# Optimization experiments

Measured on AMD Instinct MI355X. Metric: run time of the kernel, lower is better.

## Reference

```python
import jax, jax.numpy as jnp
import numpy as np

B, C, O, K, H, W = 32, 256, 256, 7, 31, 31


def _unfold(x, k):
    """Extract kxk sliding windows (stride 1, no padding, no dilation).

    x: [B, C, H, W] -> patches [B, C, k, k, Ho, Wo]
    """
    _, _, h, w = x.shape
    ho, wo = h - k + 1, w - k + 1
    # fixed small loop over k*k window offsets (k=7 -> 49 cheap slices)
    rows = []
    for i in range(k):
        cols = [x[:, :, i:i + ho, j:j + wo] for j in range(k)]
        rows.append(jnp.stack(cols, axis=2))  # [B, C, k, Ho, Wo]
    return jnp.stack(rows, axis=2)  # [B, C, k, k, Ho, Wo]


def setup_inputs() -> dict:
    key = jax.random.key(0)
    k1, k2, k3, k4 = jax.random.split(key, 4)
    x = jax.random.normal(k1, (B, C, H, W), dtype=jnp.float32)
    kernel = jax.random.normal(k2, (B, C, K, K), dtype=jnp.float32)
    weight = jax.random.normal(k3, (O, C, K, K), dtype=jnp.float32) * 0.02
    bias = jax.random.normal(k4, (O,), dtype=jnp.float32) * 0.02
    return {"x": x, "kernel": kernel, "weight": weight, "bias": bias}


def reference(x, kernel, weight, bias):
    k = weight.shape[-1]
    patches = _unfold(x, k)  # [B, C, k, k, Ho, Wo]
    # fused: (patches * kernel[..., None, None]) contracted with weight
    # torch: einsum('ijklmn,ojkl->iomn', patches * kernel_view, weight)
    out = jnp.einsum('bcklhw,bckl,ockl->bohw', patches, kernel, weight)
    out = out + bias[None, :, None, None]
    return out
```

## Files before the change

### kernel.cpp

```cpp
#include <hip/hip_runtime.h>
#include <hip/hip_fp16.h>

typedef _Float16 half8 __attribute__((ext_vector_type(8)));
typedef __attribute__((ext_vector_type(4)))  float floatx4;
typedef __attribute__((ext_vector_type(16))) float floatx16;

#define BB 32
#define CC 256
#define OO 256
#define KS 7
#define HH 31
#define WW 31
#define HO 25
#define PP 625
#define SS 49

#define SLAB_PITCH 40
#define SLAB_ROWS  310
#define P_TILE 64
#define NPX 10
#define KPD 20

#define WT4_ELEMS  ((size_t)SS * 8 * 2 * CC * 16)
#define WT4_BYTES  (WT4_ELEMS * 2)

static __device__ __forceinline__ unsigned pk2h(float lo, float hi) {
    __half2 h = __floats2half2_rn(lo, hi);
    unsigned r;
    __builtin_memcpy(&r, &h, sizeof(r));
    return r;
}
static __device__ __forceinline__ unsigned mulh2(unsigned a, unsigned b) {
    __half2 x, y;
    __builtin_memcpy(&x, &a, 4); __builtin_memcpy(&y, &b, 4);
    __half2 r = __hmul2(x, y);
    unsigned u;
    __builtin_memcpy(&u, &r, 4);
    return u;
}
static __device__ __forceinline__ half8 mod8(uint4 w, uint4 k) {
    uint4 r;
    r.x = mulh2(w.x, k.x); r.y = mulh2(w.y, k.y);
    r.z = mulh2(w.z, k.z); r.w = mulh2(w.w, k.w);
    return __builtin_bit_cast(half8, r);
}

__global__ __launch_bounds__(256) void repack_w(const float* __restrict__ w,
                                                unsigned short* __restrict__ wt4) {
    const int bid = blockIdx.x;
    const int s = bid >> 3, cb = bid & 7;
    const int o = threadIdx.x;
    const float* src = w + ((size_t)o * CC + cb * 32) * SS + s;
    float v[32];
#pragma unroll
    for (int ci = 0; ci < 32; ++ci) v[ci] = src[(size_t)ci * SS];
#pragma unroll
    for (int kh = 0; kh < 2; ++kh) {
        unsigned short* dst = wt4 + ((size_t)bid * 2 + kh) * (CC * 16) + o * 16;
        uint4 p0, p1;
        p0.x = pk2h(v[kh*16+0], v[kh*16+1]);  p0.y = pk2h(v[kh*16+2], v[kh*16+3]);
        p0.z = pk2h(v[kh*16+4], v[kh*16+5]);  p0.w = pk2h(v[kh*16+6], v[kh*16+7]);
        p1.x = pk2h(v[kh*16+8], v[kh*16+9]);  p1.y = pk2h(v[kh*16+10], v[kh*16+11]);
        p1.z = pk2h(v[kh*16+12], v[kh*16+13]); p1.w = pk2h(v[kh*16+14], v[kh*16+15]);
        *(uint4*)(dst)     = p0;
        *(uint4*)(dst + 8) = p1;
    }
}

__global__ __launch_bounds__(256, 4) void dwconv_fused(
        const float* __restrict__ x, const unsigned short* __restrict__ wt4,
        const float* __restrict__ kern, const float* __restrict__ bias,
        float* __restrict__ out) {
    __shared__ unsigned short slab[SLAB_ROWS * SLAB_PITCH];
    __shared__ unsigned klds[SS * KPD];

    const int tid = threadIdx.x;
    const int id = blockIdx.x;
    const int oy = id & 1;
    const int m = id >> 1;
    const int b = m / NPX, px = m - (m / NPX) * NPX;

    const int p0 = px * P_TILE;
    const int h0 = p0 / HO;
    const int pmax = (p0 + P_TILE - 1 < PP - 1) ? p0 + P_TILE - 1 : PP - 1;
    const int rows = pmax / HO - h0 + 7;
    const int npos = rows * WW;

    const int lane = tid & 63, wid = tid >> 6;
    const int l32 = lane & 31, half = lane >> 5;

    int bOff[2];
#pragma unroll
    for (int ph = 0; ph < 2; ++ph) {
        int p = p0 + ph * 32 + l32;
        if (p > PP - 1) p = PP - 1;
        int h = p / HO, ww_ = p - h * HO;
        bOff[ph] = ((h - h0) * WW + ww_) * SLAB_PITCH + half * 8;
    }

    const unsigned short* wbase = wt4
        + (size_t)(oy * 128 + wid * 32 + l32) * 16 + half * 8;

    floatx16 acc[2];
#pragma unroll
    for (int ph = 0; ph < 2; ++ph)
#pragma unroll
        for (int rr = 0; rr < 16; ++rr) acc[ph][rr] = 0.f;

    for (int cb = 0; cb < 8; ++cb) {
        __syncthreads();
        {
            const float* xsrc = x + ((size_t)(b * CC + cb * 32 + wid * 8)) * (HH * WW)
                                  + h0 * WW;
#pragma unroll
            for (int it = 0; it < 5; ++it) {
                int pos = lane + it * 64;
                if (pos < npos) {
                    float v[8];
#pragma unroll
                    for (int j = 0; j < 8; ++j) v[j] = xsrc[j * (HH * WW) + pos];
                    uint4 pkt;
                    pkt.x = pk2h(v[0], v[1]); pkt.y = pk2h(v[2], v[3]);
                    pkt.z = pk2h(v[4], v[5]); pkt.w = pk2h(v[6], v[7]);
                    *(uint4*)(slab + pos * SLAB_PITCH + wid * 8) = pkt;
                }
            }
        }
        {
            const float* ksrc = kern + ((size_t)(b * CC + cb * 32)) * SS;
#pragma unroll
            for (int it = 0; it < 4; ++it) {
                int f = tid + it * 256;
                if (f < 16 * SS) {
                    int s = f >> 4, pr = f & 15;
                    float v0 = ksrc[(size_t)(pr * 2) * SS + s];
                    float v1 = ksrc[(size_t)(pr * 2 + 1) * SS + s];
                    klds[s * KPD + pr] = pk2h(v0, v1);
                }
            }
        }
        __syncthreads();

        const unsigned short* aptr = wbase + (size_t)cb * 8192;
        uint4 a0k0 = *(const uint4*)(aptr);
        uint4 a0k1 = *(const uint4*)(aptr + 4096);
        uint4 a1k0 = *(const uint4*)(aptr + 65536);
        uint4 a1k1 = *(const uint4*)(aptr + 65536 + 4096);

        int kk = 0, ll = 0;
        for (int si = 0; si < SS; ++si) {
            uint4 n0, n1;
            if (si + 2 < SS) {
                const unsigned short* p2 = aptr + 2 * 65536;
                n0 = *(const uint4*)(p2);
                n1 = *(const uint4*)(p2 + 4096);
            } else {
                n0 = a1k0; n1 = a1k1;
            }

            uint4 kv0 = *(const uint4*)(klds + si * KPD + half * 4);
            uint4 kv1 = *(const uint4*)(klds + si * KPD + 8 + half * 4);

            const unsigned short* slabS = slab + (kk * WW + ll) * SLAB_PITCH;
            half8 b00 = *(const half8*)(slabS + bOff[0]);
            half8 b01 = *(const half8*)(slabS + bOff[0] + 16);
            half8 b10 = *(const half8*)(slabS + bOff[1]);
            half8 b11 = *(const half8*)(slabS + bOff[1] + 16);

            half8 a0 = mod8(a0k0, kv0);
            half8 a1 = mod8(a0k1, kv1);

            acc[0] = __builtin_amdgcn_mfma_f32_32x32x16_f16(a0, b00, acc[0], 0, 0, 0);
            acc[1] = __builtin_amdgcn_mfma_f32_32x32x16_f16(a0, b10, acc[1], 0, 0, 0);
            acc[0] = __builtin_amdgcn_mfma_f32_32x32x16_f16(a1, b01, acc[0], 0, 0, 0);
            acc[1] = __builtin_amdgcn_mfma_f32_32x32x16_f16(a1, b11, acc[1], 0, 0, 0);

            a0k0 = a1k0; a0k1 = a1k1; a1k0 = n0; a1k1 = n1;
            aptr += 65536;
            if (++ll == KS) { ll = 0; ++kk; }
        }
    }

    const int ow0 = oy * 128 + wid * 32;
#pragma unroll
    for (int c = 0; c < 4; ++c) {
        const int ob = ow0 + c * 8 + 4 * half;
        const float4 bv = *(const float4*)(bias + ob);
#pragma unroll
        for (int ph = 0; ph < 2; ++ph) {
            const int p = p0 + ph * 32 + l32;
            if (p < PP) {
                out[((size_t)(b * OO + ob + 0)) * PP + p] = acc[ph][4*c+0] + bv.x;
                out[((size_t)(b * OO + ob + 1)) * PP + p] = acc[ph][4*c+1] + bv.y;
                out[((size_t)(b * OO + ob + 2)) * PP + p] = acc[ph][4*c+2] + bv.z;
                out[((size_t)(b * OO + ob + 3)) * PP + p] = acc[ph][4*c+3] + bv.w;
            }
        }
    }
}

__global__ __launch_bounds__(256) void dwconv_naive(
        const float* __restrict__ x, const float* __restrict__ kern,
        const float* __restrict__ w, const float* __restrict__ bias,
        float* __restrict__ out) {
    const int idx = blockIdx.x * 256 + threadIdx.x;
    if (idx >= BB * OO * PP) return;
    const int p = idx % PP;
    const int o = (idx / PP) % OO;
    const int b = idx / (PP * OO);
    const int h = p / HO;
    const int wq = p - h * HO;
    float acc = 0.f;
    for (int c = 0; c < CC; ++c) {
        const float* xp = x + ((size_t)(b * CC + c)) * (HH * WW) + h * WW + wq;
        const float* kp = kern + ((size_t)b * CC + c) * SS;
        const float* wp = w + ((size_t)o * CC + c) * SS;
#pragma unroll
        for (int s = 0; s < SS; ++s) {
            const int kk = s / KS;
            const int ll = s - kk * KS;
            acc += xp[kk * WW + ll] * kp[s] * wp[s];
        }
    }
    out[idx] = acc + bias[o];
}

extern "C" void kernel_launch(void* const* d_in, const int* in_sizes, int n_in,
                              void* d_out, int out_size, void* d_ws, size_t ws_size,
                              hipStream_t stream) {
    const float* x    = (const float*)d_in[0];
    const float* kern = (const float*)d_in[1];
    const float* w    = (const float*)d_in[2];
    const float* bias = (const float*)d_in[3];
    float* out = (float*)d_out;

    if (ws_size >= WT4_BYTES) {
        unsigned short* wt4 = (unsigned short*)d_ws;
        repack_w<<<dim3(SS * 8), dim3(256), 0, stream>>>(w, wt4);
        dwconv_fused<<<dim3(640), dim3(256), 0, stream>>>(x, wt4, kern, bias, out);
    } else {
        const int total = BB * OO * PP;
        dwconv_naive<<<dim3((total + 255) / 256), dim3(256), 0, stream>>>(
            x, kern, w, bias, out);
    }
}
```

Before: 292.8 us.

## Split the 49 kernel taps across wave groups with an LDS reduction, using 512-thread blocks

Blocks grow to 512 threads (8 waves). Each wave covers 64 outputs by 32 pixels instead of 32 by 64, and the 49 spatial taps are split between two wave groups (25 and 24). A two-round LDS reduction then combines the partial accumulators before the bias add and store. The slab pitch shrinks to 36 and the weight register prefetch pipeline is removed. The aim is more waves in flight and shorter serial MFMA chains, at the cost of an extra reduction, more barriers, and no weight prefetch (weights are now loaded directly each tap).

```diff
diff --git a/kernel.cpp b/kernel.cpp
--- a/kernel.cpp
+++ b/kernel.cpp
@@ -15,7 +15,7 @@
 #define PP 625
 #define SS 49
 
-#define SLAB_PITCH 40
+#define SLAB_PITCH 36
 #define SLAB_ROWS  310
 #define P_TILE 64
 #define NPX 10
@@ -67,7 +67,7 @@
     }
 }
 
-__global__ __launch_bounds__(256, 4) void dwconv_fused(
+__global__ __launch_bounds__(512, 6) void dwconv_fused(
         const float* __restrict__ x, const unsigned short* __restrict__ wt4,
         const float* __restrict__ kern, const float* __restrict__ bias,
         float* __restrict__ out) {
@@ -87,50 +87,53 @@
     const int npos = rows * WW;
 
     const int lane = tid & 63, wid = tid >> 6;
+    const int wo = wid & 1, wp = (wid >> 1) & 1, kw = wid >> 2;
     const int l32 = lane & 31, half = lane >> 5;
 
-    int bOff[2];
-#pragma unroll
-    for (int ph = 0; ph < 2; ++ph) {
-        int p = p0 + ph * 32 + l32;
+    int bOff;
+    {
+        int p = p0 + wp * 32 + l32;
         if (p > PP - 1) p = PP - 1;
         int h = p / HO, ww_ = p - h * HO;
-        bOff[ph] = ((h - h0) * WW + ww_) * SLAB_PITCH + half * 8;
-    }
+        bOff = ((h - h0) * WW + ww_) * SLAB_PITCH + half * 8;
+    }
+
+    const int s0 = kw ? 25 : 0;
+    const int ns = kw ? 24 : 25;
 
     const unsigned short* wbase = wt4
-        + (size_t)(oy * 128 + wid * 32 + l32) * 16 + half * 8;
+        + (size_t)(oy * 128 + wo * 64 + l32) * 16 + half * 8;
 
     floatx16 acc[2];
 #pragma unroll
-    for (int ph = 0; ph < 2; ++ph)
-#pragma unroll
-        for (int rr = 0; rr < 16; ++rr) acc[ph][rr] = 0.f;
+    for (int oh = 0; oh < 2; ++oh)
+#pragma unroll
+        for (int rr = 0; rr < 16; ++rr) acc[oh][rr] = 0.f;
 
     for (int cb = 0; cb < 8; ++cb) {
         __syncthreads();
         {
-            const float* xsrc = x + ((size_t)(b * CC + cb * 32 + wid * 8)) * (HH * WW)
+            const float* xsrc = x + ((size_t)(b * CC + cb * 32 + wid * 4)) * (HH * WW)
                                   + h0 * WW;
 #pragma unroll
             for (int it = 0; it < 5; ++it) {
                 int pos = lane + it * 64;
                 if (pos < npos) {
-                    float v[8];
-#pragma unroll
-                    for (int j = 0; j < 8; ++j) v[j] = xsrc[j * (HH * WW) + pos];
-                    uint4 pkt;
-                    pkt.x = pk2h(v[0], v[1]); pkt.y = pk2h(v[2], v[3]);
-                    pkt.z = pk2h(v[4], v[5]); pkt.w = pk2h(v[6], v[7]);
-                    *(uint4*)(slab + pos * SLAB_PITCH + wid * 8) = pkt;
+                    float v0 = xsrc[pos];
+                    float v1 = xsrc[(size_t)(HH * WW) + pos];
+                    float v2 = xsrc[(size_t)(2 * HH * WW) + pos];
+                    float v3 = xsrc[(size_t)(3 * HH * WW) + pos];
+                    uint2 pkt;
+                    pkt.x = pk2h(v0, v1); pkt.y = pk2h(v2, v3);
+                    *(uint2*)(slab + pos * SLAB_PITCH + wid * 4) = pkt;
                 }
             }
         }
         {
             const float* ksrc = kern + ((size_t)(b * CC + cb * 32)) * SS;
 #pragma unroll
-            for (int it = 0; it < 4; ++it) {
-                int f = tid + it * 256;
+            for (int it = 0; it < 2; ++it) {
+                int f = tid + it * 512;
                 if (f < 16 * SS) {
                     int s = f >> 4, pr = f & 15;
                     float v0 = ksrc[(size_t)(pr * 2) * SS + s];
@@ -141,60 +144,69 @@
         }
         __syncthreads();
 
-        const unsigned short* aptr = wbase + (size_t)cb * 8192;
-        uint4 a0k0 = *(const uint4*)(aptr);
-        uint4 a0k1 = *(const uint4*)(aptr + 4096);
-        uint4 a1k0 = *(const uint4*)(aptr + 65536);
-        uint4 a1k1 = *(const uint4*)(aptr + 65536 + 4096);
-
-        int kk = 0, ll = 0;
-        for (int si = 0; si < SS; ++si) {
-            uint4 n0, n1;
-            if (si + 2 < SS) {
-                const unsigned short* p2 = aptr + 2 * 65536;
-                n0 = *(const uint4*)(p2);
-                n1 = *(const uint4*)(p2 + 4096);
-            } else {
-                n0 = a1k0; n1 = a1k1;
-            }
-
-            uint4 kv0 = *(const uint4*)(klds + si * KPD + half * 4);
-            uint4 kv1 = *(const uint4*)(klds + si * KPD + 8 + half * 4);
+        const unsigned short* aptr = wbase + (size_t)(s0 * 8 + cb) * 8192;
+
+        int kk = kw ? 3 : 0, ll = kw ? 4 : 0;
+        for (int si = 0; si < ns; ++si) {
+            uint4 wa0 = *(const uint4*)(aptr);
+            uint4 wa1 = *(const uint4*)(aptr + 512);
+            uint4 wa2 = *(const uint4*)(aptr + 4096);
+            uint4 wa3 = *(const uint4*)(aptr + 4608);
+
+            const unsigned* kp = klds + (size_t)(s0 + si) * KPD;
+            uint4 kv0 = *(const uint4*)(kp + half * 4);
+            uint4 kv1 = *(const uint4*)(kp + 8 + half * 4);
 
             const unsigned short* slabS = slab + (kk * WW + ll) * SLAB_PITCH;
-            half8 b00 = *(const half8*)(slabS + bOff[0]);
-            half8 b01 = *(const half8*)(slabS + bOff[0] + 16);
-            half8 b10 = *(const half8*)(slabS + bOff[1]);
-            half8 b11 = *(const half8*)(slabS + bOff[1] + 16);
-
-            half8 a0 = mod8(a0k0, kv0);
-            half8 a1 = mod8(a0k1, kv1);
-
-            acc[0] = __builtin_amdgcn_mfma_f32_32x32x16_f16(a0, b00, acc[0], 0, 0, 0);
-            acc[1] = __builtin_amdgcn_mfma_f32_32x32x16_f16(a0, b10, acc[1], 0, 0, 0);
-            acc[0] = __builtin_amdgcn_mfma_f32_32x32x16_f16(a1, b01, acc[0], 0, 0, 0);
-            acc[1] = __builtin_amdgcn_mfma_f32_32x32x16_f16(a1, b11, acc[1], 0, 0, 0);
-
-            a0k0 = a1k0; a0k1 = a1k1; a1k0 = n0; a1k1 = n1;
+            half8 b0 = *(const half8*)(slabS + bOff);
+            half8 b1 = *(const half8*)(slabS + bOff + 16);
+
+            half8 a0 = mod8(wa0, kv0);
+            half8 a1 = mod8(wa1, kv0);
+            half8 a2 = mod8(wa2, kv1);
+            half8 a3 = mod8(wa3, kv1);
+
+            acc[0] = __builtin_amdgcn_mfma_f32_32x32x16_f16(a0, b0, acc[0], 0, 0, 0);
+            acc[1] = __builtin_amdgcn_mfma_f32_32x32x16_f16(a1, b0, acc[1], 0, 0, 0);
+            acc[0] = __builtin_amdgcn_mfma_f32_32x32x16_f16(a2, b1, acc[0], 0, 0, 0);
+            acc[1] = __builtin_amdgcn_mfma_f32_32x32x16_f16(a3, b1, acc[1], 0, 0, 0);
+
             aptr += 65536;
             if (++ll == KS) { ll = 0; ++kk; }
         }
     }
 
-    const int ow0 = oy * 128 + wid * 32;
-#pragma unroll
-    for (int c = 0; c < 4; ++c) {
-        const int ob = ow0 + c * 8 + 4 * half;
-        const float4 bv = *(const float4*)(bias + ob);
-#pragma unroll
-        for (int ph = 0; ph < 2; ++ph) {
-            const int p = p0 + ph * 32 + l32;
-            if (p < PP) {
-                out[((size_t)(b * OO + ob + 0)) * PP + p] = acc[ph][4*c+0] + bv.x;
-                out[((size_t)(b * OO + ob + 1)) * PP + p] = acc[ph][4*c+1] + bv.y;
-                out[((size_t)(b * OO + ob + 2)) * PP + p] = acc[ph][4*c+2] + bv.z;
-                out[((size_t)(b * OO + ob + 3)) * PP + p] = acc[ph][4*c+3] + bv.w;
-            }
+    float* red = (float*)slab;
+    for (int round = 0; round < 2; ++round) {
+        __syncthreads();
+        if (kw == 1 && wp == round) {
+#pragma unroll
+            for (int oh = 0; oh < 2; ++oh)
+#pragma unroll
+                for (int c = 0; c < 4; ++c) {
+                    floatx4 v4 = {acc[oh][4*c+0], acc[oh][4*c+1],
+                                  acc[oh][4*c+2], acc[oh][4*c+3]};
+                    *(floatx4*)(red + wo * 2176 + l32 * 68 + oh * 32 + c * 8 + 4 * half) = v4;
+                }
+        }
+        __syncthreads();
+        if (kw == 0 && wp == round) {
+            const int pout = p0 + wp * 32 + l32;
+#pragma unroll
+            for (int oh = 0; oh < 2; ++oh)
+#pragma unroll
+                for (int c = 0; c < 4; ++c) {
+                    const int ob = oy * 128 + wo * 64 + oh * 32 + c * 8 + 4 * half;
+                    const float4 bv = *(const float4*)(bias + ob);
+                    floatx4 v4 = *(const floatx4*)(red + wo * 2176 + l32 * 68
+                                                   + oh * 32 + c * 8 + 4 * half);
+                    if (pout < PP) {
+                        out[((size_t)(b * OO + ob + 0)) * PP + pout] = acc[oh][4*c+0] + v4[0] + bv.x;
+                        out[((size_t)(b * OO + ob + 1)) * PP + pout] = acc[oh][4*c+1] + v4[1] + bv.y;
+                        out[((size_t)(b * OO + ob + 2)) * PP + pout] = acc[oh][4*c+2] + v4[2] + bv.z;
+                        out[((size_t)(b * OO + ob + 3)) * PP + pout] = acc[oh][4*c+3] + v4[3] + bv.w;
+                    }
+                }
         }
     }
 }
@@ -237,7 +249,7 @@
     if (ws_size >= WT4_BYTES) {
         unsigned short* wt4 = (unsigned short*)d_ws;
         repack_w<<<dim3(SS * 8), dim3(256), 0, stream>>>(w, wt4);
-        dwconv_fused<<<dim3(640), dim3(256), 0, stream>>>(x, wt4, kern, bias, out);
+        dwconv_fused<<<dim3(640), dim3(512), 0, stream>>>(x, wt4, kern, bias, out);
     } else {
         const int total = BB * OO * PP;
         dwconv_naive<<<dim3((total + 255) / 256), dim3(256), 0, stream>>>(
```

Result: slower. 414.7 us (+41.6%).

## Retile conv to 128-pixel by 32-output blocks and pre-pack x to fp16

Applied to the files above, without the earlier changes.

Adds a pack_x pre-pass that converts x to fp16 in workspace, so the main kernel loads half-width data and skips the per-block conversion. The block tile changes from 64 pixels × 128 outputs (two accumulators per wave) to 128 pixels × 32 outputs (one accumulator per wave), with 1280 blocks and a larger, narrower-pitch slab. The aim is more blocks and higher occupancy from fewer registers. The cost is an extra kernel launch, extra x traffic through workspace, and more redundant staging of x and kern because eight output tiles now each load the same slab.

```diff
diff --git a/kernel.cpp b/kernel.cpp
--- a/kernel.cpp
+++ b/kernel.cpp
@@ -15,14 +15,16 @@
 #define PP 625
 #define SS 49
 
-#define SLAB_PITCH 40
-#define SLAB_ROWS  310
-#define P_TILE 64
-#define NPX 10
+#define SLAB_PITCH 36
+#define SLAB_ROWS  372
+#define P_TILE 128
+#define NPX 5
 #define KPD 20
 
 #define WT4_ELEMS  ((size_t)SS * 8 * 2 * CC * 16)
 #define WT4_BYTES  (WT4_ELEMS * 2)
+#define X16_ELEMS  ((size_t)BB * CC * HH * WW)
+#define X16_BYTES  (X16_ELEMS * 2)
 
 static __device__ __forceinline__ unsigned pk2h(float lo, float hi) {
     __half2 h = __floats2half2_rn(lo, hi);
@@ -67,8 +69,18 @@
     }
 }
 
-__global__ __launch_bounds__(256, 4) void dwconv_fused(
-        const float* __restrict__ x, const unsigned short* __restrict__ wt4,
+__global__ __launch_bounds__(256) void pack_x(const float* __restrict__ x,
+                                              unsigned short* __restrict__ x16) {
+    const size_t i4 = ((size_t)blockIdx.x * 256 + threadIdx.x) * 4;
+    float4 v = *(const float4*)(x + i4);
+    uint2 p;
+    p.x = pk2h(v.x, v.y); p.y = pk2h(v.z, v.w);
+    *(uint2*)(x16 + i4) = p;
+}
+
+__global__ __launch_bounds__(256, 5) void dwconv_fused(
+        const unsigned short* __restrict__ x16,
+        const unsigned short* __restrict__ wt4,
         const float* __restrict__ kern, const float* __restrict__ bias,
         float* __restrict__ out) {
     __shared__ unsigned short slab[SLAB_ROWS * SLAB_PITCH];
@@ -76,8 +88,8 @@
 
     const int tid = threadIdx.x;
     const int id = blockIdx.x;
-    const int oy = id & 1;
-    const int m = id >> 1;
+    const int oy = id & 7;
+    const int m = id >> 3;
     const int b = m / NPX, px = m - (m / NPX) * NPX;
 
     const int p0 = px * P_TILE;
@@ -89,39 +101,37 @@
     const int lane = tid & 63, wid = tid >> 6;
     const int l32 = lane & 31, half = lane >> 5;
 
-    int bOff[2];
-#pragma unroll
-    for (int ph = 0; ph < 2; ++ph) {
-        int p = p0 + ph * 32 + l32;
+    int bOff;
+    {
+        int p = p0 + wid * 32 + l32;
         if (p > PP - 1) p = PP - 1;
         int h = p / HO, ww_ = p - h * HO;
-        bOff[ph] = ((h - h0) * WW + ww_) * SLAB_PITCH + half * 8;
-    }
-
-    const unsigned short* wbase = wt4
-        + (size_t)(oy * 128 + wid * 32 + l32) * 16 + half * 8;
-
-    floatx16 acc[2];
-#pragma unroll
-    for (int ph = 0; ph < 2; ++ph)
-#pragma unroll
-        for (int rr = 0; rr < 16; ++rr) acc[ph][rr] = 0.f;
+        bOff = ((h - h0) * WW + ww_) * SLAB_PITCH + half * 8;
+    }
+
+    const unsigned short* wbase = wt4 + (size_t)(oy * 32 + l32) * 16 + half * 8;
+
+    floatx16 acc;
+#pragma unroll
+    for (int rr = 0; rr < 16; ++rr) acc[rr] = 0.f;
 
     for (int cb = 0; cb < 8; ++cb) {
         __syncthreads();
         {
-            const float* xsrc = x + ((size_t)(b * CC + cb * 32 + wid * 8)) * (HH * WW)
-                                  + h0 * WW;
-#pragma unroll
-            for (int it = 0; it < 5; ++it) {
+            const unsigned short* xsrc = x16
+                + ((size_t)(b * CC + cb * 32 + wid * 8)) * (HH * WW) + h0 * WW;
+#pragma unroll
+            for (int it = 0; it < 6; ++it) {
                 int pos = lane + it * 64;
                 if (pos < npos) {
-                    float v[8];
+                    unsigned short v[8];
 #pragma unroll
                     for (int j = 0; j < 8; ++j) v[j] = xsrc[j * (HH * WW) + pos];
                     uint4 pkt;
-                    pkt.x = pk2h(v[0], v[1]); pkt.y = pk2h(v[2], v[3]);
-                    pkt.z = pk2h(v[4], v[5]); pkt.w = pk2h(v[6], v[7]);
+                    pkt.x = (unsigned)v[0] | ((unsigned)v[1] << 16);
+                    pkt.y = (unsigned)v[2] | ((unsigned)v[3] << 16);
+                    pkt.z = (unsigned)v[4] | ((unsigned)v[5] << 16);
+                    pkt.w = (unsigned)v[6] | ((unsigned)v[7] << 16);
                     *(uint4*)(slab + pos * SLAB_PITCH + wid * 8) = pkt;
                 }
             }
@@ -158,22 +168,19 @@
                 n0 = a1k0; n1 = a1k1;
             }
 
-            uint4 kv0 = *(const uint4*)(klds + si * KPD + half * 4);
-            uint4 kv1 = *(const uint4*)(klds + si * KPD + 8 + half * 4);
+            const unsigned* kp = klds + (size_t)si * KPD;
+            uint4 kv0 = *(const uint4*)(kp + half * 4);
+            uint4 kv1 = *(const uint4*)(kp + 8 + half * 4);
 
             const unsigned short* slabS = slab + (kk * WW + ll) * SLAB_PITCH;
-            half8 b00 = *(const half8*)(slabS + bOff[0]);
-            half8 b01 = *(const half8*)(slabS + bOff[0] + 16);
-            half8 b10 = *(const half8*)(slabS + bOff[1]);
-            half8 b11 = *(const half8*)(slabS + bOff[1] + 16);
+            half8 b0 = *(const half8*)(slabS + bOff);
+            half8 b1 = *(const half8*)(slabS + bOff + 16);
 
             half8 a0 = mod8(a0k0, kv0);
             half8 a1 = mod8(a0k1, kv1);
 
-            acc[0] = __builtin_amdgcn_mfma_f32_32x32x16_f16(a0, b00, acc[0], 0, 0, 0);
-            acc[1] = __builtin_amdgcn_mfma_f32_32x32x16_f16(a0, b10, acc[1], 0, 0, 0);
-            acc[0] = __builtin_amdgcn_mfma_f32_32x32x16_f16(a1, b01, acc[0], 0, 0, 0);
-            acc[1] = __builtin_amdgcn_mfma_f32_32x32x16_f16(a1, b11, acc[1], 0, 0, 0);
+            acc = __builtin_amdgcn_mfma_f32_32x32x16_f16(a0, b0, acc, 0, 0, 0);
+            acc = __builtin_amdgcn_mfma_f32_32x32x16_f16(a1, b1, acc, 0, 0, 0);
 
             a0k0 = a1k0; a0k1 = a1k1; a1k0 = n0; a1k1 = n1;
             aptr += 65536;
@@ -181,20 +188,16 @@
         }
     }
 
-    const int ow0 = oy * 128 + wid * 32;
-#pragma unroll
-    for (int c = 0; c < 4; ++c) {
-        const int ob = ow0 + c * 8 + 4 * half;
-        const float4 bv = *(const float4*)(bias + ob);
-#pragma unroll
-        for (int ph = 0; ph < 2; ++ph) {
-            const int p = p0 + ph * 32 + l32;
-            if (p < PP) {
-                out[((size_t)(b * OO + ob + 0)) * PP + p] = acc[ph][4*c+0] + bv.x;
-                out[((size_t)(b * OO + ob + 1)) * PP + p] = acc[ph][4*c+1] + bv.y;
-                out[((size_t)(b * OO + ob + 2)) * PP + p] = acc[ph][4*c+2] + bv.z;
-                out[((size_t)(b * OO + ob + 3)) * PP + p] = acc[ph][4*c+3] + bv.w;
-            }
+    const int pout = p0 + wid * 32 + l32;
+    if (pout < PP) {
+#pragma unroll
+        for (int c = 0; c < 4; ++c) {
+            const int ob = oy * 32 + c * 8 + 4 * half;
+            const float4 bv = *(const float4*)(bias + ob);
+            out[((size_t)(b * OO + ob + 0)) * PP + pout] = acc[4*c+0] + bv.x;
+            out[((size_t)(b * OO + ob + 1)) * PP + pout] = acc[4*c+1] + bv.y;
+            out[((size_t)(b * OO + ob + 2)) * PP + pout] = acc[4*c+2] + bv.z;
+            out[((size_t)(b * OO + ob + 3)) * PP + pout] = acc[4*c+3] + bv.w;
         }
     }
 }
@@ -234,10 +237,12 @@
     const float* bias = (const float*)d_in[3];
     float* out = (float*)d_out;
 
-    if (ws_size >= WT4_BYTES) {
+    if (ws_size >= WT4_BYTES + X16_BYTES) {
         unsigned short* wt4 = (unsigned short*)d_ws;
+        unsigned short* x16 = (unsigned short*)((char*)d_ws + WT4_BYTES);
         repack_w<<<dim3(SS * 8), dim3(256), 0, stream>>>(w, wt4);
-        dwconv_fused<<<dim3(640), dim3(256), 0, stream>>>(x, wt4, kern, bias, out);
+        pack_x<<<dim3((unsigned)(X16_ELEMS / 4 / 256)), dim3(256), 0, stream>>>(x, x16);
+        dwconv_fused<<<dim3(1280), dim3(256), 0, stream>>>(x16, wt4, kern, bias, out);
     } else {
         const int total = BB * OO * PP;
         dwconv_naive<<<dim3((total + 255) / 256), dim3(256), 0, stream>>>(
```

Measured after the change: 582.5 us. 98.9% more time.

## Split 49 kernel taps across waves with LDS reduction and 64-output tiles

Applied to the files above, without the earlier changes.

Each block now covers 64 outputs × 64 positions, and its four waves split the 49 spatial taps (13/12/12/12) instead of splitting output channels. Partial accumulators are combined through a serialized LDS reduction before the bias add and store. The grid doubles to 1280 blocks, the block order is swizzled, the slab pitch shrinks to 36, and the occupancy hint drops to 3. This trades extra LDS reduction, barriers and accumulator registers for more parallelism and shared slab reads per weight fragment.

```diff
diff --git a/kernel.cpp b/kernel.cpp
--- a/kernel.cpp
+++ b/kernel.cpp
@@ -15,10 +15,8 @@
 #define PP 625
 #define SS 49
 
-#define SLAB_PITCH 40
+#define SLAB_PITCH 36
 #define SLAB_ROWS  310
-#define P_TILE 64
-#define NPX 10
 #define KPD 20
 
 #define WT4_ELEMS  ((size_t)SS * 8 * 2 * CC * 16)
@@ -67,7 +65,7 @@
     }
 }
 
-__global__ __launch_bounds__(256, 4) void dwconv_fused(
+__global__ __launch_bounds__(256, 3) void dwconv_fused(
         const float* __restrict__ x, const unsigned short* __restrict__ wt4,
         const float* __restrict__ kern, const float* __restrict__ bias,
         float* __restrict__ out) {
@@ -76,17 +74,18 @@
 
     const int tid = threadIdx.x;
     const int id = blockIdx.x;
-    const int oy = id & 1;
-    const int m = id >> 1;
-    const int b = m / NPX, px = m - (m / NPX) * NPX;
-
-    const int p0 = px * P_TILE;
+    const int hi = id / 80, rem = id % 80;
+    const int px = rem >> 3;
+    const int g = hi * 8 + (rem & 7);
+    const int b = g >> 2, oy = g & 3;
+
+    const int p0 = px * 64, o0 = oy * 64;
     const int h0 = p0 / HO;
-    const int pmax = (p0 + P_TILE - 1 < PP - 1) ? p0 + P_TILE - 1 : PP - 1;
+    const int pmax = (p0 + 63 < PP - 1) ? p0 + 63 : PP - 1;
     const int rows = pmax / HO - h0 + 7;
     const int npos = rows * WW;
 
-    const int lane = tid & 63, wid = tid >> 6;
+    const int lane = tid & 63, kw = tid >> 6;
     const int l32 = lane & 31, half = lane >> 5;
 
     int bOff[2];
@@ -98,19 +97,23 @@
         bOff[ph] = ((h - h0) * WW + ww_) * SLAB_PITCH + half * 8;
     }
 
-    const unsigned short* wbase = wt4
-        + (size_t)(oy * 128 + wid * 32 + l32) * 16 + half * 8;
-
-    floatx16 acc[2];
-#pragma unroll
-    for (int ph = 0; ph < 2; ++ph)
-#pragma unroll
-        for (int rr = 0; rr < 16; ++rr) acc[ph][rr] = 0.f;
+    const int s0 = kw * 12 + (kw > 0 ? 1 : 0);
+    const int ns = kw ? 12 : 13;
+
+    const unsigned short* wbase = wt4 + (size_t)(o0 + l32) * 16 + half * 8;
+
+    floatx16 acc[2][2];
+#pragma unroll
+    for (int oh = 0; oh < 2; ++oh)
+#pragma unroll
+        for (int ph = 0; ph < 2; ++ph)
+#pragma unroll
+            for (int r = 0; r < 16; ++r) acc[oh][ph][r] = 0.f;
 
     for (int cb = 0; cb < 8; ++cb) {
         __syncthreads();
         {
-            const float* xsrc = x + ((size_t)(b * CC + cb * 32 + wid * 8)) * (HH * WW)
+            const float* xsrc = x + ((size_t)(b * CC + cb * 32 + kw * 8)) * (HH * WW)
                                   + h0 * WW;
 #pragma unroll
             for (int it = 0; it < 5; ++it) {
@@ -122,7 +125,7 @@
                     uint4 pkt;
                     pkt.x = pk2h(v[0], v[1]); pkt.y = pk2h(v[2], v[3]);
                     pkt.z = pk2h(v[4], v[5]); pkt.w = pk2h(v[6], v[7]);
-                    *(uint4*)(slab + pos * SLAB_PITCH + wid * 8) = pkt;
+                    *(uint4*)(slab + pos * SLAB_PITCH + kw * 8) = pkt;
                 }
             }
         }
@@ -141,61 +144,119 @@
         }
         __syncthreads();
 
-        const unsigned short* aptr = wbase + (size_t)cb * 8192;
-        uint4 a0k0 = *(const uint4*)(aptr);
-        uint4 a0k1 = *(const uint4*)(aptr + 4096);
-        uint4 a1k0 = *(const uint4*)(aptr + 65536);
-        uint4 a1k1 = *(const uint4*)(aptr + 65536 + 4096);
-
-        int kk = 0, ll = 0;
-        for (int si = 0; si < SS; ++si) {
-            uint4 n0, n1;
-            if (si + 2 < SS) {
-                const unsigned short* p2 = aptr + 2 * 65536;
-                n0 = *(const uint4*)(p2);
-                n1 = *(const uint4*)(p2 + 4096);
+        const unsigned short* aptr = wbase + (size_t)(s0 * 8 + cb) * 8192;
+
+        uint4 wa0 = *(const uint4*)(aptr);
+        uint4 wa1 = *(const uint4*)(aptr + 512);
+        uint4 wa2 = *(const uint4*)(aptr + 4096);
+        uint4 wa3 = *(const uint4*)(aptr + 4608);
+
+        int s = s0, kk = s0 / KS, ll = s0 - (s0 / KS) * KS;
+        for (int si = 0; si < ns; ++si) {
+            uint4 wn0, wn1, wn2, wn3;
+            if (si + 1 < ns) {
+                aptr += 65536;
+                wn0 = *(const uint4*)(aptr);
+                wn1 = *(const uint4*)(aptr + 512);
+                wn2 = *(const uint4*)(aptr + 4096);
+                wn3 = *(const uint4*)(aptr + 4608);
             } else {
-                n0 = a1k0; n1 = a1k1;
+                wn0 = wa0; wn1 = wa1; wn2 = wa2; wn3 = wa3;
             }
 
-            uint4 kv0 = *(const uint4*)(klds + si * KPD + half * 4);
-            uint4 kv1 = *(const uint4*)(klds + si * KPD + 8 + half * 4);
+            const unsigned* kp = klds + (size_t)s * KPD;
+            uint4 kv0 = *(const uint4*)(kp + half * 4);
+            uint4 kv1 = *(const uint4*)(kp + 8 + half * 4);
 
             const unsigned short* slabS = slab + (kk * WW + ll) * SLAB_PITCH;
-            half8 b00 = *(const half8*)(slabS + bOff[0]);
-            half8 b01 = *(const half8*)(slabS + bOff[0] + 16);
-            half8 b10 = *(const half8*)(slabS + bOff[1]);
-            half8 b11 = *(const half8*)(slabS + bOff[1] + 16);
-
-            half8 a0 = mod8(a0k0, kv0);
-            half8 a1 = mod8(a0k1, kv1);
-
-            acc[0] = __builtin_amdgcn_mfma_f32_32x32x16_f16(a0, b00, acc[0], 0, 0, 0);
-            acc[1] = __builtin_amdgcn_mfma_f32_32x32x16_f16(a0, b10, acc[1], 0, 0, 0);
-            acc[0] = __builtin_amdgcn_mfma_f32_32x32x16_f16(a1, b01, acc[0], 0, 0, 0);
-            acc[1] = __builtin_amdgcn_mfma_f32_32x32x16_f16(a1, b11, acc[1], 0, 0, 0);
-
-            a0k0 = a1k0; a0k1 = a1k1; a1k0 = n0; a1k1 = n1;
-            aptr += 65536;
-            if (++ll == KS) { ll = 0; ++kk; }
+            half8 sb00 = *(const half8*)(slabS + bOff[0]);
+            half8 sb01 = *(const half8*)(slabS + bOff[0] + 16);
+            half8 sb10 = *(const half8*)(slabS + bOff[1]);
+            half8 sb11 = *(const half8*)(slabS + bOff[1] + 16);
+
+            half8 a00 = mod8(wa0, kv0);
+            half8 a10 = mod8(wa1, kv0);
+            half8 a01 = mod8(wa2, kv1);
+            half8 a11 = mod8(wa3, kv1);
+
+            acc[0][0] = __builtin_amdgcn_mfma_f32_32x32x16_f16(a00, sb00, acc[0][0], 0, 0, 0);
+            acc[0][1] = __builtin_amdgcn_mfma_f32_32x32x16_f16(a00, sb10, acc[0][1], 0, 0, 0);
+            acc[1][0] = __builtin_amdgcn_mfma_f32_32x32x16_f16(a10, sb00, acc[1][0], 0, 0, 0);
+            acc[1][1] = __builtin_amdgcn_mfma_f32_32x32x16_f16(a10, sb10, acc[1][1], 0, 0, 0);
+            acc[0][0] = __builtin_amdgcn_mfma_f32_32x32x16_f16(a01, sb01, acc[0][0], 0, 0, 0);
+            acc[0][1] = __builtin_amdgcn_mfma_f32_32x32x16_f16(a01, sb11, acc[0][1], 0, 0, 0);
+            acc[1][0] = __builtin_amdgcn_mfma_f32_32x32x16_f16(a11, sb01, acc[1][0], 0, 0, 0);
+            acc[1][1] = __builtin_amdgcn_mfma_f32_32x32x16_f16(a11, sb11, acc[1][1], 0, 0, 0);
+
+            wa0 = wn0; wa1 = wn1; wa2 = wn2; wa3 = wn3;
+            ++s; if (++ll == KS) { ll = 0; ++kk; }
         }
     }
 
-    const int ow0 = oy * 128 + wid * 32;
-#pragma unroll
-    for (int c = 0; c < 4; ++c) {
-        const int ob = ow0 + c * 8 + 4 * half;
-        const float4 bv = *(const float4*)(bias + ob);
-#pragma unroll
-        for (int ph = 0; ph < 2; ++ph) {
-            const int p = p0 + ph * 32 + l32;
-            if (p < PP) {
-                out[((size_t)(b * OO + ob + 0)) * PP + p] = acc[ph][4*c+0] + bv.x;
-                out[((size_t)(b * OO + ob + 1)) * PP + p] = acc[ph][4*c+1] + bv.y;
-                out[((size_t)(b * OO + ob + 2)) * PP + p] = acc[ph][4*c+2] + bv.z;
-                out[((size_t)(b * OO + ob + 3)) * PP + p] = acc[ph][4*c+3] + bv.w;
+    float* red = (float*)slab;
+    __syncthreads();
+    if (kw == 3) {
+#pragma unroll
+        for (int oh = 0; oh < 2; ++oh)
+#pragma unroll
+            for (int ph = 0; ph < 2; ++ph)
+#pragma unroll
+                for (int c = 0; c < 4; ++c) {
+                    floatx4 v4 = {acc[oh][ph][4*c+0], acc[oh][ph][4*c+1],
+                                  acc[oh][ph][4*c+2], acc[oh][ph][4*c+3]};
+                    *(floatx4*)(red + (ph * 32 + l32) * 68 + oh * 32 + c * 8 + 4 * half) = v4;
+                }
+    }
+    __syncthreads();
+    if (kw == 2) {
+#pragma unroll
+        for (int oh = 0; oh < 2; ++oh)
+#pragma unroll
+            for (int ph = 0; ph < 2; ++ph)
+#pragma unroll
+                for (int c = 0; c < 4; ++c) {
+                    float* rp = red + (ph * 32 + l32) * 68 + oh * 32 + c * 8 + 4 * half;
+                    floatx4 v4 = *(floatx4*)rp;
+                    v4[0] += acc[oh][ph][4*c+0]; v4[1] += acc[oh][ph][4*c+1];
+                    v4[2] += acc[oh][ph][4*c+2]; v4[3] += acc[oh][ph][4*c+3];
+                    *(floatx4*)rp = v4;
+                }
+    }
+    __syncthreads();
+    if (kw == 1) {
+#pragma unroll
+        for (int oh = 0; oh < 2; ++oh)
+#pragma unroll
+            for (int ph = 0; ph < 2; ++ph)
+#pragma unroll
+                for (int c = 0; c < 4; ++c) {
+                    float* rp = red + (ph * 32 + l32) * 68 + oh * 32 + c * 8 + 4 * half;
+                    floatx4 v4 = *(floatx4*)rp;
+                    v4[0] += acc[oh][ph][4*c+0]; v4[1] += acc[oh][ph][4*c+1];
+                    v4[2] += acc[oh][ph][4*c+2]; v4[3] += acc[oh][ph][4*c+3];
+                    *(floatx4*)rp = v4;
+                }
+    }
+    __syncthreads();
+    if (kw == 0) {
+#pragma unroll
+        for (int oh = 0; oh < 2; ++oh)
+#pragma unroll
+            for (int c = 0; c < 4; ++c) {
+                const int ob = o0 + oh * 32 + c * 8 + 4 * half;
+                const float4 bv = *(const float4*)(bias + ob);
+#pragma unroll
+                for (int ph = 0; ph < 2; ++ph) {
+                    const int p = p0 + ph * 32 + l32;
+                    floatx4 v4 = *(floatx4*)(red + (ph * 32 + l32) * 68 + oh * 32 + c * 8 + 4 * half);
+                    if (p < PP) {
+                        out[((size_t)(b * OO + ob + 0)) * PP + p] = v4[0] + acc[oh][ph][4*c+0] + bv.x;
+                        out[((size_t)(b * OO + ob + 1)) * PP + p] = v4[1] + acc[oh][ph][4*c+1] + bv.y;
+                        out[((size_t)(b * OO + ob + 2)) * PP + p] = v4[2] + acc[oh][ph][4*c+2] + bv.z;
+                        out[((size_t)(b * OO + ob + 3)) * PP + p] = v4[3] + acc[oh][ph][4*c+3] + bv.w;
+                    }
+                }
             }
-        }
     }
 }
 
@@ -237,7 +298,7 @@
     if (ws_size >= WT4_BYTES) {
         unsigned short* wt4 = (unsigned short*)d_ws;
         repack_w<<<dim3(SS * 8), dim3(256), 0, stream>>>(w, wt4);
-        dwconv_fused<<<dim3(640), dim3(256), 0, stream>>>(x, wt4, kern, bias, out);
+        dwconv_fused<<<dim3(1280), dim3(256), 0, stream>>>(x, wt4, kern, bias, out);
     } else {
         const int total = BB * OO * PP;
         dwconv_naive<<<dim3((total + 255) / 256), dim3(256), 0, stream>>>(
```

Result: slower. 384.8 us (+31.4%).
